# Performance work log

Measured on AMD Instinct MI355X. Metric: run time of the kernel, lower is better.

The kernel has to match this reference:

```python
import jax, jax.numpy as jnp
import numpy as np

N = 8_000_000

def setup_inputs() -> dict:
    key = jax.random.key(0)
    k1, k2 = jax.random.split(key)
    rotation = jax.random.normal(k1, (N, 4), dtype=jnp.float32)
    # make quaternions non-degenerate (w biased positive, like identity init)
    rotation = rotation.at[:, 0].add(1.0)
    scale = jax.random.uniform(k2, (N, 3), dtype=jnp.float32) + 0.1
    return {"rotation": rotation, "scale": scale}

def _quat_to_rotmat(q):
    # q: [N,4] in (w, x, y, z) order (from_pcd sets q[:,0]=1 -> identity)
    q = q / jnp.linalg.norm(q, axis=-1, keepdims=True)
    w, x, y, z = q[:, 0], q[:, 1], q[:, 2], q[:, 3]
    R = jnp.stack([
        jnp.stack([1 - 2 * (y * y + z * z), 2 * (x * y - w * z), 2 * (x * z + w * y)], axis=-1),
        jnp.stack([2 * (x * y + w * z), 1 - 2 * (x * x + z * z), 2 * (y * z - w * x)], axis=-1),
        jnp.stack([2 * (x * z - w * y), 2 * (y * z + w * x), 1 - 2 * (x * x + y * y)], axis=-1),
    ], axis=-2)  # [N,3,3]
    return R

def reference(rotation, scale):
    # cov = (R S) (R S)^T restricted to the top-left 3x3 block
    R = _quat_to_rotmat(rotation)            # [N,3,3]
    M = R * scale[:, None, :]                # R @ diag(scale), scales columns
    cov = jnp.einsum('nij,nkj->nik', M, M)   # [N,3,3]
    return cov
```

## Files before the change

### kernel.cpp

```cpp
#include <hip/hip_runtime.h>


__global__ __launch_bounds__(256) void gauss_cov_kernel(
    const float* __restrict__ rot,
    const float* __restrict__ scl,
    float* __restrict__ out,
    int ngroups,
    int rem_base, int rem)
{
    const int stride = gridDim.x * blockDim.x;
    for (int g = blockIdx.x * blockDim.x + threadIdx.x; g < ngroups; g += stride) {
        const float4* rq = reinterpret_cast<const float4*>(rot) + 4 * (size_t)g;
        float4 q0 = rq[0], q1 = rq[1], q2 = rq[2], q3 = rq[3];
        const float4* rs = reinterpret_cast<const float4*>(scl + 12 * (size_t)g);
        float4 s0 = rs[0], s1 = rs[1], s2 = rs[2];

        float qw[4] = {q0.x, q1.x, q2.x, q3.x};
        float qx[4] = {q0.y, q1.y, q2.y, q3.y};
        float qy[4] = {q0.z, q1.z, q2.z, q3.z};
        float qz[4] = {q0.w, q1.w, q2.w, q3.w};
        float sa[4] = {s0.x, s0.w, s1.z, s2.y};
        float sb[4] = {s0.y, s1.x, s1.w, s2.z};
        float sc[4] = {s0.z, s1.y, s2.x, s2.w};

        float o[36];
        #pragma unroll
        for (int i = 0; i < 4; ++i) {
            float w = qw[i], x = qx[i], y = qy[i], z = qz[i];
            float d = w * w + x * x + y * y + z * z;
            float inv = 1.0f / sqrtf(d);
            w *= inv; x *= inv; y *= inv; z *= inv;

            float R00 = 1.f - 2.f * (y * y + z * z);
            float R01 = 2.f * (x * y - w * z);
            float R02 = 2.f * (x * z + w * y);
            float R10 = 2.f * (x * y + w * z);
            float R11 = 1.f - 2.f * (x * x + z * z);
            float R12 = 2.f * (y * z - w * x);
            float R20 = 2.f * (x * z - w * y);
            float R21 = 2.f * (y * z + w * x);
            float R22 = 1.f - 2.f * (x * x + y * y);

            float a = sa[i] * sa[i], b = sb[i] * sb[i], c = sc[i] * sc[i];

            float c00 = R00 * R00 * a + R01 * R01 * b + R02 * R02 * c;
            float c01 = R00 * R10 * a + R01 * R11 * b + R02 * R12 * c;
            float c02 = R00 * R20 * a + R01 * R21 * b + R02 * R22 * c;
            float c11 = R10 * R10 * a + R11 * R11 * b + R12 * R12 * c;
            float c12 = R10 * R20 * a + R11 * R21 * b + R12 * R22 * c;
            float c22 = R20 * R20 * a + R21 * R21 * b + R22 * R22 * c;

            float* oi = o + 9 * i;
            oi[0] = c00; oi[1] = c01; oi[2] = c02;
            oi[3] = c01; oi[4] = c11; oi[5] = c12;
            oi[6] = c02; oi[7] = c12; oi[8] = c22;
        }

        float4* o4 = reinterpret_cast<float4*>(out + 36 * (size_t)g);
        const float4* src = reinterpret_cast<const float4*>(o);
        #pragma unroll
        for (int j = 0; j < 9; ++j) o4[j] = src[j];
    }

    if (blockIdx.x == 0 && (int)threadIdx.x < rem) {
        int e = rem_base + threadIdx.x;
        float w = rot[4 * (size_t)e + 0], x = rot[4 * (size_t)e + 1];
        float y = rot[4 * (size_t)e + 2], z = rot[4 * (size_t)e + 3];
        float inv = 1.0f / sqrtf(w * w + x * x + y * y + z * z);
        w *= inv; x *= inv; y *= inv; z *= inv;
        float R00 = 1.f - 2.f * (y * y + z * z), R01 = 2.f * (x * y - w * z), R02 = 2.f * (x * z + w * y);
        float R10 = 2.f * (x * y + w * z), R11 = 1.f - 2.f * (x * x + z * z), R12 = 2.f * (y * z - w * x);
        float R20 = 2.f * (x * z - w * y), R21 = 2.f * (y * z + w * x), R22 = 1.f - 2.f * (x * x + y * y);
        float a = scl[3 * (size_t)e + 0]; a *= a;
        float b = scl[3 * (size_t)e + 1]; b *= b;
        float c = scl[3 * (size_t)e + 2]; c *= c;
        float* oi = out + 9 * (size_t)e;
        float c00 = R00 * R00 * a + R01 * R01 * b + R02 * R02 * c;
        float c01 = R00 * R10 * a + R01 * R11 * b + R02 * R12 * c;
        float c02 = R00 * R20 * a + R01 * R21 * b + R02 * R22 * c;
        float c11 = R10 * R10 * a + R11 * R11 * b + R12 * R12 * c;
        float c12 = R10 * R20 * a + R11 * R21 * b + R12 * R22 * c;
        float c22 = R20 * R20 * a + R21 * R21 * b + R22 * R22 * c;
        oi[0] = c00; oi[1] = c01; oi[2] = c02;
        oi[3] = c01; oi[4] = c11; oi[5] = c12;
        oi[6] = c02; oi[7] = c12; oi[8] = c22;
    }
}

extern "C" void kernel_launch(void* const* d_in, const int* in_sizes, int n_in,
                              void* d_out, int out_size, void* d_ws, size_t ws_size,
                              hipStream_t stream) {
    const float* rot = (const float*)d_in[0];
    const float* scl = (const float*)d_in[1];
    float* out = (float*)d_out;

    const int n = in_sizes[0] / 4;
    const int ngroups = n / 4;
    const int rem = n - 4 * ngroups;
    const int rem_base = 4 * ngroups;

    int grid = (ngroups + 255) / 256;
    if (grid > 2048) grid = 2048;
    if (grid < 1) grid = 1;

    gauss_cov_kernel<<<grid, 256, 0, stream>>>(rot, scl, out, ngroups, rem_base, rem);
}
```

Baseline: 517.2 us.

## Stage scale loads and covariance stores through shared memory for coalescing

Replaces the grid-stride loop, where each thread handled four gaussians with strided float4 loads and stores, with one gaussian per thread and one block per 256 elements. Scale values are read into shared memory with coalesced loads, and the 3x3 outputs are staged in shared memory and then written out as contiguous float4 stores. The aim is fully coalesced global traffic for this bandwidth-bound kernel. In exchange it adds two block barriers, about 12 KB of LDS per block, and a much larger grid with no grid-stride reuse.

Result: faster. 418.9 us (-19.0%).

```diff
diff --git a/kernel.cpp b/kernel.cpp
--- a/kernel.cpp
+++ b/kernel.cpp
@@ -1,89 +1,73 @@
 #include <hip/hip_runtime.h>
 
+
+constexpr int BLK = 256;
 
 __global__ __launch_bounds__(256) void gauss_cov_kernel(
     const float* __restrict__ rot,
     const float* __restrict__ scl,
     float* __restrict__ out,
-    int ngroups,
-    int rem_base, int rem)
+    int n)
 {
-    const int stride = gridDim.x * blockDim.x;
-    for (int g = blockIdx.x * blockDim.x + threadIdx.x; g < ngroups; g += stride) {
-        const float4* rq = reinterpret_cast<const float4*>(rot) + 4 * (size_t)g;
-        float4 q0 = rq[0], q1 = rq[1], q2 = rq[2], q3 = rq[3];
-        const float4* rs = reinterpret_cast<const float4*>(scl + 12 * (size_t)g);
-        float4 s0 = rs[0], s1 = rs[1], s2 = rs[2];
+    __shared__ float s_scl[3 * BLK];
+    __shared__ float s_out[9 * BLK];
 
-        float qw[4] = {q0.x, q1.x, q2.x, q3.x};
-        float qx[4] = {q0.y, q1.y, q2.y, q3.y};
-        float qy[4] = {q0.z, q1.z, q2.z, q3.z};
-        float qz[4] = {q0.w, q1.w, q2.w, q3.w};
-        float sa[4] = {s0.x, s0.w, s1.z, s2.y};
-        float sb[4] = {s0.y, s1.x, s1.w, s2.z};
-        float sc[4] = {s0.z, s1.y, s2.x, s2.w};
+    const size_t base = (size_t)blockIdx.x * BLK;
+    const int t = threadIdx.x;
+    const size_t g = base + t;
+    const int valid = (int)((n - (long long)base < BLK) ? (n - (long long)base) : BLK);
 
-        float o[36];
-        #pragma unroll
-        for (int i = 0; i < 4; ++i) {
-            float w = qw[i], x = qx[i], y = qy[i], z = qz[i];
-            float d = w * w + x * x + y * y + z * z;
-            float inv = 1.0f / sqrtf(d);
-            w *= inv; x *= inv; y *= inv; z *= inv;
+    for (int j = t; j < 3 * valid; j += BLK)
+        s_scl[j] = scl[3 * base + j];
 
-            float R00 = 1.f - 2.f * (y * y + z * z);
-            float R01 = 2.f * (x * y - w * z);
-            float R02 = 2.f * (x * z + w * y);
-            float R10 = 2.f * (x * y + w * z);
-            float R11 = 1.f - 2.f * (x * x + z * z);
-            float R12 = 2.f * (y * z - w * x);
-            float R20 = 2.f * (x * z - w * y);
-            float R21 = 2.f * (y * z + w * x);
-            float R22 = 1.f - 2.f * (x * x + y * y);
+    float4 q = make_float4(1.f, 0.f, 0.f, 0.f);
+    if (g < (size_t)n) q = reinterpret_cast<const float4*>(rot)[g];
 
-            float a = sa[i] * sa[i], b = sb[i] * sb[i], c = sc[i] * sc[i];
+    __syncthreads();
 
-            float c00 = R00 * R00 * a + R01 * R01 * b + R02 * R02 * c;
-            float c01 = R00 * R10 * a + R01 * R11 * b + R02 * R12 * c;
-            float c02 = R00 * R20 * a + R01 * R21 * b + R02 * R22 * c;
-            float c11 = R10 * R10 * a + R11 * R11 * b + R12 * R12 * c;
-            float c12 = R10 * R20 * a + R11 * R21 * b + R12 * R22 * c;
-            float c22 = R20 * R20 * a + R21 * R21 * b + R22 * R22 * c;
-
-            float* oi = o + 9 * i;
-            oi[0] = c00; oi[1] = c01; oi[2] = c02;
-            oi[3] = c01; oi[4] = c11; oi[5] = c12;
-            oi[6] = c02; oi[7] = c12; oi[8] = c22;
-        }
-
-        float4* o4 = reinterpret_cast<float4*>(out + 36 * (size_t)g);
-        const float4* src = reinterpret_cast<const float4*>(o);
-        #pragma unroll
-        for (int j = 0; j < 9; ++j) o4[j] = src[j];
-    }
-
-    if (blockIdx.x == 0 && (int)threadIdx.x < rem) {
-        int e = rem_base + threadIdx.x;
-        float w = rot[4 * (size_t)e + 0], x = rot[4 * (size_t)e + 1];
-        float y = rot[4 * (size_t)e + 2], z = rot[4 * (size_t)e + 3];
+    if (t < valid) {
+        float w = q.x, x = q.y, y = q.z, z = q.w;
         float inv = 1.0f / sqrtf(w * w + x * x + y * y + z * z);
         w *= inv; x *= inv; y *= inv; z *= inv;
-        float R00 = 1.f - 2.f * (y * y + z * z), R01 = 2.f * (x * y - w * z), R02 = 2.f * (x * z + w * y);
-        float R10 = 2.f * (x * y + w * z), R11 = 1.f - 2.f * (x * x + z * z), R12 = 2.f * (y * z - w * x);
-        float R20 = 2.f * (x * z - w * y), R21 = 2.f * (y * z + w * x), R22 = 1.f - 2.f * (x * x + y * y);
-        float a = scl[3 * (size_t)e + 0]; a *= a;
-        float b = scl[3 * (size_t)e + 1]; b *= b;
-        float c = scl[3 * (size_t)e + 2]; c *= c;
-        float* oi = out + 9 * (size_t)e;
+
+        float R00 = 1.f - 2.f * (y * y + z * z);
+        float R01 = 2.f * (x * y - w * z);
+        float R02 = 2.f * (x * z + w * y);
+        float R10 = 2.f * (x * y + w * z);
+        float R11 = 1.f - 2.f * (x * x + z * z);
+        float R12 = 2.f * (y * z - w * x);
+        float R20 = 2.f * (x * z - w * y);
+        float R21 = 2.f * (y * z + w * x);
+        float R22 = 1.f - 2.f * (x * x + y * y);
+
+        float a = s_scl[3 * t + 0]; a *= a;
+        float b = s_scl[3 * t + 1]; b *= b;
+        float c = s_scl[3 * t + 2]; c *= c;
+
         float c00 = R00 * R00 * a + R01 * R01 * b + R02 * R02 * c;
         float c01 = R00 * R10 * a + R01 * R11 * b + R02 * R12 * c;
         float c02 = R00 * R20 * a + R01 * R21 * b + R02 * R22 * c;
         float c11 = R10 * R10 * a + R11 * R11 * b + R12 * R12 * c;
         float c12 = R10 * R20 * a + R11 * R21 * b + R12 * R22 * c;
         float c22 = R20 * R20 * a + R21 * R21 * b + R22 * R22 * c;
-        oi[0] = c00; oi[1] = c01; oi[2] = c02;
-        oi[3] = c01; oi[4] = c11; oi[5] = c12;
-        oi[6] = c02; oi[7] = c12; oi[8] = c22;
+
+        float* o = s_out + 9 * t;
+        o[0] = c00; o[1] = c01; o[2] = c02;
+        o[3] = c01; o[4] = c11; o[5] = c12;
+        o[6] = c02; o[7] = c12; o[8] = c22;
+    }
+
+    __syncthreads();
+
+    if (valid == BLK) {
+        float4* ob = reinterpret_cast<float4*>(out + 9 * base);
+        const float4* sb = reinterpret_cast<const float4*>(s_out);
+        ob[t]       = sb[t];
+        ob[t + 256] = sb[t + 256];
+        if (t < 64) ob[t + 512] = sb[t + 512];
+    } else {
+        for (int j = t; j < 9 * valid; j += BLK)
+            out[9 * base + j] = s_out[j];
     }
 }
 
@@ -95,13 +79,7 @@
     float* out = (float*)d_out;
 
     const int n = in_sizes[0] / 4;
-    const int ngroups = n / 4;
-    const int rem = n - 4 * ngroups;
-    const int rem_base = 4 * ngroups;
+    const int grid = (n + BLK - 1) / BLK;
 
-    int grid = (ngroups + 255) / 256;
-    if (grid > 2048) grid = 2048;
-    if (grid < 1) grid = 1;
-
-    gauss_cov_kernel<<<grid, 256, 0, stream>>>(rot, scl, out, ngroups, rem_base, rem);
+    gauss_cov_kernel<<<grid, BLK, 0, stream>>>(rot, scl, out, n);
 }
```
